# Optimization experiments

Measured on AMD Instinct MI355X. Metric: run time of the kernel, lower is better.

The kernel has to match this reference:

```python
import jax, jax.numpy as jnp
import numpy as np

N = 100_000        # nodes
E = 3_200_000      # edges (avg degree 32)
H = 20             # hidden_channels (forced by forward body)
EH = 64            # edge_hidden_dim
EOUT = 10          # edge_output_dim (forced: 10 + EOUT == H)
THRESHOLD = 10.0


def setup_inputs() -> dict:
    key = jax.random.key(0)
    ks = jax.random.split(key, 12)
    x = jax.random.normal(ks[0], (N, 2, H), dtype=jnp.float32)
    edge_index = jax.random.randint(ks[1], (2, E), 0, N, dtype=jnp.int32)
    # distances must be in (0, threshold]
    edge_attr = jax.random.uniform(ks[2], (E, 1), dtype=jnp.float32, minval=1e-3, maxval=THRESHOLD)
    # module parameters (match torch init distributions: uniform[0,1))
    a = jax.random.uniform(ks[3], (1,), dtype=jnp.float32)
    b = jax.random.uniform(ks[4], (1,), dtype=jnp.float32) + 1.0
    gamma1 = jax.random.uniform(ks[5], (H, H), dtype=jnp.float32)
    gamma2 = jax.random.uniform(ks[6], (H, H), dtype=jnp.float32)
    bias = jax.random.uniform(ks[7], (H,), dtype=jnp.float32)
    # EdgeFeatureMLP2 params: Linear(1->EH), Linear(EH->EOUT)
    W1 = jax.random.normal(ks[8], (1, EH), dtype=jnp.float32)
    b1 = jax.random.normal(ks[9], (EH,), dtype=jnp.float32) * 0.1
    W2 = jax.random.normal(ks[10], (EH, EOUT), dtype=jnp.float32) / np.sqrt(EH)
    b2 = jax.random.normal(ks[11], (EOUT,), dtype=jnp.float32) * 0.1
    return dict(x=x, edge_index=edge_index, edge_attr=edge_attr, a=a, b=b,
                gamma1=gamma1, gamma2=gamma2, bias=bias, W1=W1, b1=b1, W2=W2, b2=b2)


def reference(x, edge_index, edge_attr, a, b, gamma1, gamma2, bias, W1, b1, W2, b2):
    src, dst = edge_index[0], edge_index[1]
    # edge MLP: Linear -> ReLU -> Linear -> ReLU
    h = jax.nn.relu(edge_attr @ W1 + b1)                    # [E, EH]
    mlp_out = jax.nn.relu(h @ W2 + b2)                      # [E, EOUT]
    # one-hot distance bucket: int(d / (threshold/10)), clipped to 9
    idx = jnp.minimum((edge_attr[:, 0] / (THRESHOLD / 10.0)).astype(jnp.int32), 9)
    one_hot = jax.nn.one_hot(idx, 10, dtype=edge_attr.dtype)  # [E, 10]
    comb = jnp.concatenate([one_hot, mlp_out], axis=1)      # [E, 20]
    # w_tilde: per-edge features normalized by the sum over all edges from the source node
    sum_w = jax.ops.segment_sum(comb, src, num_segments=N)  # [N, 20]
    sw = sum_w[src]                                         # [E, 20]
    nz = sw != 0
    w_tilde = jnp.where(nz, comb / jnp.where(nz, sw, 1.0), 0.01)
    # rho weighting: |a*h_j - (1-a)*h_j'|^b, elementwise over the 20-dim slot-0 features
    rho = jnp.abs(a * x[src, 0] - (1.0 - a) * x[dst, 0]) ** b  # [E, 20]
    sum_feat = jax.ops.segment_sum(rho * w_tilde, src, num_segments=N)  # [N, 20]
    # node update: relu(gamma1 @ x_j + gamma2 @ sum_feat_j + bias)
    out0 = jax.nn.relu(x[:, 0] @ gamma1.T + sum_feat @ gamma2.T + bias)  # [N, 20]
    return jnp.stack([out0, sum_feat], axis=1)              # [N, 2, 20]
```

## Files before the change

### kernel.cpp

```cpp
#include <hip/hip_runtime.h>

#define NN 100000
#define NE 3200000
#define HD 20
#define EHD 64
#define EOUTD 10
#define TBINS 4096

#define EPB 8192
#define NBLKS1 391
#define NBINS1 256
#define N1 (NBINS1 * NBLKS1)
#define NBUCK 196
#define WIN 4096
#define WPB 6
#define NWIN (NBUCK * WPB)
#define N2 (NBUCK * 512 * WPB)
#define KMASK 0x1FFFF

__global__ void scan1_kernel(int* __restrict__ data, int* __restrict__ bsum, int n) {
    __shared__ int s[1024];
    int t = threadIdx.x;
    int i = blockIdx.x * 1024 + t;
    int v = (i < n) ? data[i] : 0;
    s[t] = v;
    __syncthreads();
    for (int off = 1; off < 1024; off <<= 1) {
        int add = (t >= off) ? s[t - off] : 0;
        __syncthreads();
        s[t] += add;
        __syncthreads();
    }
    if (i < n) data[i] = s[t] - v;
    if (t == 1023) bsum[blockIdx.x] = s[t];
}

__global__ void scan3f_kernel(int* __restrict__ data, const int* __restrict__ bsum,
                              int nb, int n) {
    __shared__ int s[1024];
    int t = threadIdx.x;
    int v = (t < nb) ? bsum[t] : 0;
    s[t] = v;
    __syncthreads();
    for (int off = 1; off < 1024; off <<= 1) {
        int add = (t >= off) ? s[t - off] : 0;
        __syncthreads();
        s[t] += add;
        __syncthreads();
    }
    __syncthreads();
    int i = blockIdx.x * 1024 + t;
    if (i < n) data[i] += s[i >> 10] - ((i >> 10) < nb ? bsum[i >> 10] : 0);
}

__global__ void scan3bf_kernel(int* __restrict__ data, const int* __restrict__ bsum,
                               int nb, int* __restrict__ offsets) {
    __shared__ int s[1024];
    int t = threadIdx.x;
    int v = (t < nb) ? bsum[t] : 0;
    s[t] = v;
    __syncthreads();
    for (int off = 1; off < 1024; off <<= 1) {
        int add = (t >= off) ? s[t - off] : 0;
        __syncthreads();
        s[t] += add;
        __syncthreads();
    }
    __syncthreads();
    int i = blockIdx.x * 1024 + t;
    if (i >= N2) return;
    int blk = i >> 10;
    int vv = data[i] + s[blk] - (blk < nb ? bsum[blk] : 0);
    data[i] = vv;
    if (i % WPB == 0) {
        int nbidx = i / WPB;
        if (nbidx <= NN) offsets[nbidx] = vv;
    }
}

__global__ void hist1_kernel(const int* __restrict__ ei, int* __restrict__ counts1) {
    __shared__ int h[NBINS1];
    int t = threadIdx.x;
    if (t < NBINS1) h[t] = 0;
    __syncthreads();
    int base = blockIdx.x * EPB;
    for (int j = t; j < EPB; j += 1024) {
        int e = base + j;
        if (e < NE) atomicAdd(&h[ei[e] >> 9], 1);
    }
    __syncthreads();
    if (t < NBINS1) counts1[t * NBLKS1 + blockIdx.x] = h[t];
}

__global__ void scatter1_kernel(const int* __restrict__ ei,
                                const float* __restrict__ ea,
                                const int* __restrict__ counts1s,
                                int2* __restrict__ pk1) {
    __shared__ int cur[NBINS1];
    int t = threadIdx.x;
    if (t < NBINS1) cur[t] = counts1s[t * NBLKS1 + blockIdx.x];
    __syncthreads();
    int base = blockIdx.x * EPB;
    for (int j = t; j < EPB; j += 1024) {
        int e = base + j;
        if (e >= NE) break;
        int src = ei[e];
        int pos = atomicAdd(&cur[src >> 9], 1);
        int2 pk;
        pk.x = ei[NE + e] | ((src & 511) << 17);
        pk.y = __float_as_int(ea[e]);
        pk1[pos] = pk;
    }
}

__global__ void hist2_kernel(const int2* __restrict__ pk1,
                             const int* __restrict__ counts1s,
                             int* __restrict__ M2) {
    __shared__ int h[512];
    int t = threadIdx.x;
    h[t] = 0; h[t + 256] = 0;
    __syncthreads();
    int b = blockIdx.x / WPB, w = blockIdx.x % WPB;
    int bstart = counts1s[b * NBLKS1];
    int bend   = counts1s[(b + 1) * NBLKS1];
    int start = bstart + w * WIN;
    int end = (start + WIN < bend) ? (start + WIN) : bend;
    for (int i = start + t; i < end; i += 256)
        atomicAdd(&h[(pk1[i].x >> 17) & 511], 1);
    __syncthreads();
    M2[((b * 512) + t) * WPB + w]       = h[t];
    M2[((b * 512) + t + 256) * WPB + w] = h[t + 256];
}

__global__ void scatter2_kernel(const int2* __restrict__ pk1,
                                const int* __restrict__ counts1s,
                                const int* __restrict__ M2s,
                                int2* __restrict__ csr_pk) {
    __shared__ int cur[512];
    int t = threadIdx.x;
    int b = blockIdx.x / WPB, w = blockIdx.x % WPB;
    cur[t]       = M2s[((b * 512) + t) * WPB + w];
    cur[t + 256] = M2s[((b * 512) + t + 256) * WPB + w];
    __syncthreads();
    int bstart = counts1s[b * NBLKS1];
    int bend   = counts1s[(b + 1) * NBLKS1];
    int start = bstart + w * WIN;
    int end = (start + WIN < bend) ? (start + WIN) : bend;
    for (int i = start + t; i < end; i += 256) {
        int2 pk = pk1[i];
        int pos = atomicAdd(&cur[(pk.x >> 17) & 511], 1);
        float d = __int_as_float(pk.y);
        int idx = (int)d; if (idx > 9) idx = 9;
        float u = d * ((float)TBINS / 10.0f);
        int ti = (int)u; if (ti > TBINS - 1) ti = TBINS - 1;
        float fr = u - (float)ti;
        int fr16 = (int)(fr * 65536.0f); if (fr16 > 65535) fr16 = 65535;
        pk.x &= KMASK;
        pk.y = fr16 | (ti << 16) | (idx << 28);
        csr_pk[pos] = pk;
    }
}

__global__ void prep_kernel(const float* __restrict__ W1,
                            const float* __restrict__ b1,
                            const float* __restrict__ W2,
                            const float* __restrict__ b2,
                            const float* __restrict__ x,
                            unsigned short* __restrict__ tab,
                            int* __restrict__ xbf2) {
    const int TBLK = (TBINS + 255) / 256;
    auto bf16 = [](float f) -> unsigned int {
        unsigned int u = __float_as_uint(f);
        return (u + 0x7fffu + ((u >> 16) & 1u)) >> 16;
    };
    if (blockIdx.x < TBLK) {
        int i = blockIdx.x * 256 + threadIdx.x;
        if (i >= TBINS) return;
        float m0[EOUTD], m1[EOUTD];
        float d0 = (float)i * (10.0f / (float)TBINS);
        float d1 = (float)(i + 1) * (10.0f / (float)TBINS);
        #pragma unroll
        for (int j = 0; j < EOUTD; ++j) { m0[j] = b2[j]; m1[j] = b2[j]; }
        for (int k = 0; k < EHD; ++k) {
            float h0 = fmaxf(fmaf(d0, W1[k], b1[k]), 0.0f);
            float h1 = fmaxf(fmaf(d1, W1[k], b1[k]), 0.0f);
            #pragma unroll
            for (int j = 0; j < EOUTD; ++j) {
                m0[j] = fmaf(h0, W2[k * EOUTD + j], m0[j]);
                m1[j] = fmaf(h1, W2[k * EOUTD + j], m1[j]);
            }
        }
        unsigned short* row = tab + (size_t)i * 32;
        #pragma unroll
        for (int j = 0; j < EOUTD; ++j) {
            row[2 * j]     = (unsigned short)bf16(m0[j]);
            row[2 * j + 1] = (unsigned short)bf16(m1[j] - m0[j]);
        }
        #pragma unroll
        for (int j = 20; j < 32; ++j) row[j] = 0;
    } else {
        int t = (blockIdx.x - TBLK) * 256 + threadIdx.x;
        if (t >= NN * 16) return;
        int node = t >> 4, k = t & 15;
        int v = 0;
        if (k < 10) {
            v = (int)(bf16(x[(size_t)node * 2 * HD + k])
                      | (bf16(x[(size_t)node * 2 * HD + k + 10]) << 16));
        }
        xbf2[t] = v;
    }
}

__launch_bounds__(256)
__global__ void node_kernel(const int* __restrict__ offsets,
                            const int2* __restrict__ csr_pk,
                            const float* __restrict__ x,
                            const int* __restrict__ xbf2,
                            const unsigned short* __restrict__ tab,
                            const float* __restrict__ pa,
                            const float* __restrict__ pb,
                            const float* __restrict__ g1,
                            const float* __restrict__ g2,
                            const float* __restrict__ bias,
                            float* __restrict__ out) {
    int tid  = threadIdx.x;
    int wave = tid >> 6;
    int lane = tid & 63;
    int sub  = lane / 10;
    int fk   = lane - sub * 10;
    int node = blockIdx.x * 24 + wave * 6 + sub;
    bool active = (sub < 6) && (node < NN);

    float a = pa[0], bb = pb[0];
    float oma = 1.0f - a;

    int off0 = 0, deg = 0;
    float xs_lo = 0.0f, xs_hi = 0.0f, axs_lo = 0.0f, axs_hi = 0.0f;
    if (active) {
        off0 = offsets[node];
        deg  = offsets[node + 1] - off0;
        xs_lo = x[(size_t)node * 2 * HD + fk];
        xs_hi = x[(size_t)node * 2 * HD + fk + 10];
        axs_lo = a * xs_lo;
        axs_hi = a * xs_hi;
    }

    float S0a = 0.0f, S1a = 0.0f, Sra = 0.0f;
    float S0b = 0.0f, S1b = 0.0f, Srb = 0.0f;

    auto process = [&](int dst, int dy) {
        int ti  = (dy >> 16) & 0xFFF;
        int idx = (dy >> 28) & 0xF;
        float fr = (float)(dy & 0xFFFF) * (1.0f / 65536.0f);
        unsigned int xw = (unsigned int)xbf2[(((size_t)(unsigned int)dst) << 4) + fk];
        unsigned int tv = *(const unsigned int*)(tab + (((size_t)ti) << 5) + fk * 2);
        float xd_lo = __uint_as_float(xw << 16);
        float xd_hi = __uint_as_float(xw & 0xffff0000u);
        float t0 = fmaf(-oma, xd_lo, axs_lo);
        float t1 = fmaf(-oma, xd_hi, axs_hi);
        float r0 = (t0 != 0.0f)
            ? __builtin_amdgcn_exp2f(bb * __builtin_amdgcn_logf(fabsf(t0))) : 0.0f;
        float r1 = (t1 != 0.0f)
            ? __builtin_amdgcn_exp2f(bb * __builtin_amdgcn_logf(fabsf(t1))) : 0.0f;
        Sra += r0; Srb += r1;
        float c0 = (fk == idx) ? 1.0f : 0.0f;
        float val = __uint_as_float(tv << 16);
        float del = __uint_as_float(tv & 0xffff0000u);
        float c1 = fmaxf(fmaf(fr, del, val), 0.0f);
        S0a += c0; S1a = fmaf(r0, c0, S1a);
        S0b += c1; S1b = fmaf(r1, c1, S1b);
    };

    for (int base = 0; base < deg; base += 10) {
        int nchunk = deg - base; if (nchunk > 10) nchunk = 10;
        int idxc = off0 + base + ((fk < nchunk) ? fk : (nchunk - 1));
        int2 pk = csr_pk[idxc];
        int dstv = pk.x, dbits = pk.y;
        int jj = 0;
        for (; jj + 1 < nchunk; jj += 2) {
            int dA = __shfl(dstv, sub * 10 + jj, 64);
            int bA = __shfl(dbits, sub * 10 + jj, 64);
            int dB = __shfl(dstv, sub * 10 + jj + 1, 64);
            int bB = __shfl(dbits, sub * 10 + jj + 1, 64);
            process(dA, bA);
            process(dB, bB);
        }
        if (jj < nchunk) {
            int dA = __shfl(dstv, sub * 10 + jj, 64);
            int bA = __shfl(dbits, sub * 10 + jj, 64);
            process(dA, bA);
        }
    }

    float sf_lo = (S0a != 0.0f) ? (S1a / S0a) : (0.01f * Sra);
    float sf_hi = (S0b != 0.0f) ? (S1b / S0b) : (0.01f * Srb);

    if (active) {
        float acc0 = bias[fk];
        float acc1 = bias[fk + 10];
        const float* g1r0 = g1 + fk * HD;
        const float* g1r1 = g1 + (fk + 10) * HD;
        const float* g2r0 = g2 + fk * HD;
        const float* g2r1 = g2 + (fk + 10) * HD;
        #pragma unroll
        for (int j = 0; j < 10; ++j) {
            int sl = sub * 10 + j;
            float xj  = __shfl(xs_lo, sl, 64);
            float xj1 = __shfl(xs_hi, sl, 64);
            float sj  = __shfl(sf_lo, sl, 64);
            float sj1 = __shfl(sf_hi, sl, 64);
            acc0 = fmaf(xj, g1r0[j], acc0);  acc0 = fmaf(xj1, g1r0[j + 10], acc0);
            acc0 = fmaf(sj, g2r0[j], acc0);  acc0 = fmaf(sj1, g2r0[j + 10], acc0);
            acc1 = fmaf(xj, g1r1[j], acc1);  acc1 = fmaf(xj1, g1r1[j + 10], acc1);
            acc1 = fmaf(sj, g2r1[j], acc1);  acc1 = fmaf(sj1, g2r1[j + 10], acc1);
        }
        float* op = out + (size_t)node * 2 * HD;
        op[fk]          = fmaxf(acc0, 0.0f);
        op[fk + 10]     = fmaxf(acc1, 0.0f);
        op[HD + fk]     = sf_lo;
        op[HD + fk + 10] = sf_hi;
    }
}

extern "C" void kernel_launch(void* const* d_in, const int* in_sizes, int n_in,
                              void* d_out, int out_size, void* d_ws, size_t ws_size,
                              hipStream_t stream) {
    const float* x    = (const float*)d_in[0];
    const int*   ei   = (const int*)d_in[1];
    const float* ea   = (const float*)d_in[2];
    const float* pa   = (const float*)d_in[3];
    const float* pb   = (const float*)d_in[4];
    const float* g1   = (const float*)d_in[5];
    const float* g2   = (const float*)d_in[6];
    const float* bias = (const float*)d_in[7];
    const float* W1   = (const float*)d_in[8];
    const float* b1   = (const float*)d_in[9];
    const float* W2   = (const float*)d_in[10];
    const float* b2   = (const float*)d_in[11];
    float* out = (float*)d_out;

    char* ws = (char*)d_ws;
    int*   counts1 = (int*)ws;     ws += ((size_t)N1 * 4 + 127) / 128 * 128;
    int*   bsum1   = (int*)ws;     ws += (1024 * 4 + 127) / 128 * 128;
    int*   M2      = (int*)ws;     ws += ((size_t)N2 * 4 + 127) / 128 * 128;
    int*   bsum2   = (int*)ws;     ws += (1024 * 4 + 127) / 128 * 128;
    int*   offsets = (int*)ws;     ws += ((size_t)(NN + 1) * 4 + 127) / 128 * 128;
    int2*  pk1     = (int2*)ws;    ws += (size_t)NE * 8;
    int2*  csr_pk  = (int2*)ws;    ws += (size_t)NE * 8;
    unsigned short* tab = (unsigned short*)ws;   ws += ((size_t)TBINS * 32 * 2 + 127) / 128 * 128;
    int*   xbf2    = (int*)ws;     ws += ((size_t)NN * 16 * 4 + 127) / 128 * 128;

    const int TBLK = (TBINS + 255) / 256;
    prep_kernel<<<TBLK + (NN * 16 + 255) / 256, 256, 0, stream>>>(W1, b1, W2, b2, x,
                                                                  tab, xbf2);

    const int nb1 = (N1 + 1023) / 1024;
    hist1_kernel<<<NBLKS1, 1024, 0, stream>>>(ei, counts1);
    scan1_kernel<<<nb1, 1024, 0, stream>>>(counts1, bsum1, N1);
    scan3f_kernel<<<nb1, 1024, 0, stream>>>(counts1, bsum1, nb1, N1);
    scatter1_kernel<<<NBLKS1, 1024, 0, stream>>>(ei, ea, counts1, pk1);

    const int nb2 = (N2 + 1023) / 1024;
    hist2_kernel<<<NWIN, 256, 0, stream>>>(pk1, counts1, M2);
    scan1_kernel<<<nb2, 1024, 0, stream>>>(M2, bsum2, N2);
    scan3bf_kernel<<<nb2, 1024, 0, stream>>>(M2, bsum2, nb2, offsets);
    scatter2_kernel<<<NWIN, 256, 0, stream>>>(pk1, counts1, M2, csr_pk);

    node_kernel<<<(NN + 23) / 24, 256, 0, stream>>>(offsets, csr_pk, x, xbf2, tab,
                                                    pa, pb, g1, g2, bias, out);
}
```

Before: 174.4 us.

## Locally sort edges by bucket in shared memory before scatter1 writes

Scatter1 now stages each block's edges in shared memory, computes a per-block bucket prefix, and reorders them by bucket locally, so the global writes to pk1 land in contiguous runs instead of scattered 8-byte stores. Blocks are shrunk to 2048 edges and 512 threads, which increases the block count and the size of the counts1 histogram and scan. The end-of-bucket bound for the last bucket is now guarded explicitly. The cost is extra shared memory (about 35KB per block), more syncs, and a larger scan.

Measured after the change: 174.5 us. About the same (+0.0%).

```diff
diff --git a/kernel.cpp b/kernel.cpp
--- a/kernel.cpp
+++ b/kernel.cpp
@@ -7,8 +7,8 @@
 #define EOUTD 10
 #define TBINS 4096
 
-#define EPB 8192
-#define NBLKS1 391
+#define EPB 2048
+#define NBLKS1 1563
 #define NBINS1 256
 #define N1 (NBINS1 * NBLKS1)
 #define NBUCK 196
@@ -84,7 +84,7 @@
     if (t < NBINS1) h[t] = 0;
     __syncthreads();
     int base = blockIdx.x * EPB;
-    for (int j = t; j < EPB; j += 1024) {
+    for (int j = t; j < EPB; j += 512) {
         int e = base + j;
         if (e < NE) atomicAdd(&h[ei[e] >> 9], 1);
     }
@@ -96,20 +96,60 @@
                                 const float* __restrict__ ea,
                                 const int* __restrict__ counts1s,
                                 int2* __restrict__ pk1) {
-    __shared__ int cur[NBINS1];
-    int t = threadIdx.x;
-    if (t < NBINS1) cur[t] = counts1s[t * NBLKS1 + blockIdx.x];
-    __syncthreads();
-    int base = blockIdx.x * EPB;
-    for (int j = t; j < EPB; j += 1024) {
+    __shared__ int2 rec[EPB];
+    __shared__ int2 srt[EPB];
+    __shared__ unsigned char bin8[EPB];
+    __shared__ unsigned char bin8s[EPB];
+    __shared__ int hh[NBINS1];
+    __shared__ int hbase[NBINS1];
+    int t = threadIdx.x;
+    int blk = blockIdx.x;
+    int base = blk * EPB;
+    int n = NE - base; if (n > EPB) n = EPB;
+
+    if (t < NBINS1) hh[t] = 0;
+    __syncthreads();
+
+    for (int j = t; j < n; j += 512) {
         int e = base + j;
-        if (e >= NE) break;
         int src = ei[e];
-        int pos = atomicAdd(&cur[src >> 9], 1);
+        int b = src >> 9;
         int2 pk;
         pk.x = ei[NE + e] | ((src & 511) << 17);
         pk.y = __float_as_int(ea[e]);
-        pk1[pos] = pk;
+        rec[j] = pk;
+        bin8[j] = (unsigned char)b;
+        atomicAdd(&hh[b], 1);
+    }
+    __syncthreads();
+
+    int orig = (t < NBINS1) ? hh[t] : 0;
+    if (t < NBINS1) hbase[t] = orig;
+    __syncthreads();
+    for (int off = 1; off < NBINS1; off <<= 1) {
+        int add = (t < NBINS1 && t >= off) ? hbase[t - off] : 0;
+        __syncthreads();
+        if (t < NBINS1) hbase[t] += add;
+        __syncthreads();
+    }
+    if (t < NBINS1) {
+        hbase[t] -= orig;
+        hh[t] = hbase[t];
+    }
+    __syncthreads();
+
+    for (int j = t; j < n; j += 512) {
+        int b = bin8[j];
+        int pos = atomicAdd(&hh[b], 1);
+        srt[pos] = rec[j];
+        bin8s[pos] = (unsigned char)b;
+    }
+    __syncthreads();
+
+    for (int j = t; j < n; j += 512) {
+        int b = bin8s[j];
+        int gpos = counts1s[b * NBLKS1 + blk] + (j - hbase[b]);
+        pk1[gpos] = srt[j];
     }
 }
 
@@ -122,7 +162,9 @@
     __syncthreads();
     int b = blockIdx.x / WPB, w = blockIdx.x % WPB;
     int bstart = counts1s[b * NBLKS1];
-    int bend   = counts1s[(b + 1) * NBLKS1];
+    int bend;
+    if (b + 1 < NBINS1) bend = counts1s[(b + 1) * NBLKS1];
+    else bend = NE;
     int start = bstart + w * WIN;
     int end = (start + WIN < bend) ? (start + WIN) : bend;
     for (int i = start + t; i < end; i += 256)
@@ -143,7 +185,9 @@
     cur[t + 256] = M2s[((b * 512) + t + 256) * WPB + w];
     __syncthreads();
     int bstart = counts1s[b * NBLKS1];
-    int bend   = counts1s[(b + 1) * NBLKS1];
+    int bend;
+    if (b + 1 < NBINS1) bend = counts1s[(b + 1) * NBLKS1];
+    else bend = NE;
     int start = bstart + w * WIN;
     int end = (start + WIN < bend) ? (start + WIN) : bend;
     for (int i = start + t; i < end; i += 256) {
@@ -355,10 +399,10 @@
                                                                   tab, xbf2);
 
     const int nb1 = (N1 + 1023) / 1024;
-    hist1_kernel<<<NBLKS1, 1024, 0, stream>>>(ei, counts1);
+    hist1_kernel<<<NBLKS1, 512, 0, stream>>>(ei, counts1);
     scan1_kernel<<<nb1, 1024, 0, stream>>>(counts1, bsum1, N1);
     scan3f_kernel<<<nb1, 1024, 0, stream>>>(counts1, bsum1, nb1, N1);
-    scatter1_kernel<<<NBLKS1, 1024, 0, stream>>>(ei, ea, counts1, pk1);
+    scatter1_kernel<<<NBLKS1, 512, 0, stream>>>(ei, ea, counts1, pk1);
 
     const int nb2 = (N2 + 1023) / 1024;
     hist2_kernel<<<NWIN, 256, 0, stream>>>(pk1, counts1, M2);
```
